# Performance work log

Hardware: AMD Instinct MI355X
Metric: run time of the kernel (lower is better)

## Reference

```python
import jax, jax.numpy as jnp
import numpy as np

B, T, D = 2, 2048, 1024
NH, NKV, HD = 16, 4, 64
KD = NKV * HD          # 256
PD = 16                # rope partial dim (rotated dims)
RANK = 8
ALPHA = 1.0
ROPE_BASE = 10000.0


def setup_inputs() -> dict:
    key = jax.random.key(0)
    ks = jax.random.split(key, 10)
    s = 0.02
    return {
        "x":      jax.random.normal(ks[0], (B, T, D), jnp.float32),
        "Wq":     jax.random.normal(ks[1], (D, D), jnp.float32) * s,
        "Wk":     jax.random.normal(ks[2], (KD, D), jnp.float32) * s,
        "Wv":     jax.random.normal(ks[3], (KD, D), jnp.float32) * s,
        "Wproj":  jax.random.normal(ks[4], (D, D), jnp.float32) * s,
        "q_gain": jnp.full((NH,), 5.25, jnp.float32),
        "Aq":     jax.random.normal(ks[5], (RANK, D), jnp.float32) * s,
        "Bq":     jax.random.normal(ks[6], (D, RANK), jnp.float32) * s,
        "Av":     jax.random.normal(ks[7], (RANK, D), jnp.float32) * s,
        "Bv":     jax.random.normal(ks[8], (KD, RANK), jnp.float32) * s,
    }


def _rms_norm(x):
    # F.rms_norm with no weight: x / sqrt(mean(x^2) + eps), eps = dtype machine eps
    eps = jnp.finfo(x.dtype).eps
    return x * jax.lax.rsqrt(jnp.mean(x * x, axis=-1, keepdims=True) + eps)


def _rope_partial(x, cos, sin, pd):
    # x: [B, T, H, HD]; rotate first pd dims (half/half), pass rest through
    h = pd // 2
    x1, x2, rest = x[..., :h], x[..., h:pd], x[..., pd:]
    c = cos[None, :, None, :]  # [1, T, 1, h]
    s = sin[None, :, None, :]
    return jnp.concatenate([x1 * c + x2 * s, -x2 * c + x1 * s, rest], axis=-1)


def reference(x, Wq, Wk, Wv, Wproj, q_gain, Aq, Bq, Av, Bv):
    # projections + per-step LoRA on Q and V (output = alpha * B(A(x)))
    q = x @ Wq.T + ALPHA * ((x @ Aq.T) @ Bq.T)          # [B,T,D]
    k = x @ Wk.T                                        # [B,T,KD]
    v = x @ Wv.T + ALPHA * ((x @ Av.T) @ Bv.T)          # [B,T,KD]

    q = _rms_norm(q.reshape(B, T, NH, HD))
    k = _rms_norm(k.reshape(B, T, NKV, HD))
    v = v.reshape(B, T, NKV, HD)

    # partial RoPE tables: [T, PD//2]
    inv = 1.0 / (ROPE_BASE ** (jnp.arange(0, PD, 2, dtype=jnp.float32) / PD))
    freqs = jnp.arange(T, dtype=jnp.float32)[:, None] * inv[None, :]
    cos, sin = jnp.cos(freqs), jnp.sin(freqs)
    q = _rope_partial(q, cos, sin, PD)
    k = _rope_partial(k, cos, sin, PD)

    # learned per-head QK gain on queries
    q = q * q_gain[None, None, :, None]

    # GQA: repeat-interleave kv heads to NH
    g = NH // NKV
    kf = jnp.repeat(k, g, axis=2)  # [B,T,NH,HD]
    vf = jnp.repeat(v, g, axis=2)

    scale = 1.0 / np.float32(np.sqrt(HD))
    scores = jnp.einsum('bqhd,bkhd->bhqk', q, kf) * scale  # [B,NH,T,T]
    causal = jnp.tril(jnp.ones((T, T), bool))
    scores = jnp.where(causal[None, None], scores, -jnp.inf)
    p = jax.nn.softmax(scores, axis=-1)
    y = jnp.einsum('bhqk,bkhd->bqhd', p, vf).reshape(B, T, D)
    return y @ Wproj.T
```

## Files before the change

kernel.cpp:

```cpp
#include <hip/hip_runtime.h>

#define Tn   2048
#define Dn   1024
#define KDn  256
#define NHn  16
#define NKVn 4
#define Rn   4096

typedef short bf16x8 __attribute__((ext_vector_type(8)));
typedef float f32x4  __attribute__((ext_vector_type(4)));
typedef const __attribute__((address_space(1))) unsigned* gas_p;
typedef __attribute__((address_space(3))) unsigned* las_p;

__device__ unsigned short g_q[(size_t)Rn * Dn];
__device__ unsigned short g_k[(size_t)Rn * KDn];
__device__ unsigned short g_vt[(size_t)2 * NKVn * 64 * Tn];
__device__ unsigned short g_y[(size_t)Rn * Dn];
__device__ unsigned short g_xb[(size_t)Rn * Dn];
__device__ unsigned short g_wq[(size_t)Dn * Dn];
__device__ unsigned short g_wk[(size_t)KDn * Dn];
__device__ unsigned short g_wv[(size_t)KDn * Dn];
__device__ unsigned short g_wp[(size_t)Dn * Dn];
__device__ float g_tq[Rn * 8];
__device__ float g_tv[Rn * 8];

static __device__ __forceinline__ float bf2f(unsigned short u) {
    return __uint_as_float(((unsigned)u) << 16);
}
static __device__ __forceinline__ unsigned short f2bf(float f) {
    unsigned u = __float_as_uint(f);
    u += 0x7fffu + ((u >> 16) & 1u);
    return (unsigned short)(u >> 16);
}
static __device__ __forceinline__ unsigned pk2bf(float a, float b) {
    return (unsigned)f2bf(a) | ((unsigned)f2bf(b) << 16);
}
static __device__ __forceinline__ unsigned cvtpk(float a, float b) {
    unsigned r;
    asm("v_cvt_pk_bf16_f32 %0, %1, %2" : "=v"(r) : "v"(a), "v"(b));
    return r;
}
static __device__ __forceinline__ float wave_sum(float s) {
    #pragma unroll
    for (int off = 32; off; off >>= 1) s += __shfl_xor(s, off);
    return s;
}

__global__ __launch_bounds__(256)
void lora_tmp(const float* __restrict__ x,
              const float* __restrict__ Aq,
              const float* __restrict__ Av) {
    int tid = threadIdx.x, wave = tid >> 6, lane = tid & 63;
    int row = blockIdx.x * 4 + wave;
    const float4* xr = (const float4*)(x + (size_t)row * Dn);
    uint2* xbo = (uint2*)g_xb + (size_t)row * (Dn / 4);
    float aq[8], av[8];
    #pragma unroll
    for (int r = 0; r < 8; r++) { aq[r] = 0.f; av[r] = 0.f; }
    for (int it = 0; it < Dn / 256; it++) {
        int j = it * 64 + lane;
        float4 xv = xr[j];
        xbo[j] = make_uint2(pk2bf(xv.x, xv.y), pk2bf(xv.z, xv.w));
        #pragma unroll
        for (int r = 0; r < 8; r++) {
            float4 a4 = ((const float4*)(Aq + (size_t)r * Dn))[j];
            aq[r] += xv.x * a4.x + xv.y * a4.y + xv.z * a4.z + xv.w * a4.w;
        }
        #pragma unroll
        for (int r = 0; r < 8; r++) {
            float4 a4 = ((const float4*)(Av + (size_t)r * Dn))[j];
            av[r] += xv.x * a4.x + xv.y * a4.y + xv.z * a4.z + xv.w * a4.w;
        }
    }
    #pragma unroll
    for (int r = 0; r < 8; r++) { aq[r] = wave_sum(aq[r]); av[r] = wave_sum(av[r]); }
    if (lane == 0) {
        #pragma unroll
        for (int r = 0; r < 8; r++) { g_tq[row * 8 + r] = aq[r]; g_tv[row * 8 + r] = av[r]; }
    }
}

#define NQ4 (Dn * Dn / 4)
#define NK4 (KDn * Dn / 4)
__global__ __launch_bounds__(256)
void cast_w(const float* __restrict__ Wq, const float* __restrict__ Wk,
            const float* __restrict__ Wv, const float* __restrict__ Wp) {
    int i = blockIdx.x * 256 + threadIdx.x;
    const float* src; unsigned short* dst; int o;
    if      (i < NQ4)                 { src = Wq; dst = g_wq; o = i; }
    else if (i < NQ4 + NK4)           { src = Wk; dst = g_wk; o = i - NQ4; }
    else if (i < NQ4 + 2 * NK4)       { src = Wv; dst = g_wv; o = i - NQ4 - NK4; }
    else                              { src = Wp; dst = g_wp; o = i - NQ4 - 2 * NK4; }
    float4 v = ((const float4*)src)[o];
    ((uint2*)dst)[o] = make_uint2(pk2bf(v.x, v.y), pk2bf(v.z, v.w));
}

template<int MODE>
__global__ __launch_bounds__(256, 2)
void gemm_bt(float* __restrict__ Cout, const float* __restrict__ BqL,
             const float* __restrict__ BvL, const float* __restrict__ qgain,
             int M, int K) {
    const unsigned short* A = (MODE == 0) ? g_xb : g_y;

    int gx = gridDim.x;
    int flat = blockIdx.y * gx + blockIdx.x;
    int cpx = (gx * gridDim.y) >> 3;
    int flat2 = (flat & 7) * cpx + (flat >> 3);
    int n0 = (flat2 % gx) * 64, m0 = (flat2 / gx) * 128;

    const unsigned short* W;
    int wroff, region;
    if (MODE == 0) {
        if (n0 < 1024)      { W = g_wq; wroff = n0;        region = 0; }
        else if (n0 < 1280) { W = g_wk; wroff = n0 - 1024; region = 1; }
        else                { W = g_wv; wroff = n0 - 1280; region = 2; }
    } else { W = g_wp; wroff = n0; region = 3; }

    __shared__ __align__(16) unsigned short SM[24576];
    int tid = threadIdx.x;
    int w = tid >> 6, lane = tid & 63;
    int m_ = lane & 15, quad = lane >> 4;

    int lrow = lane >> 3, lseg = (lane & 7) * 8;
    const unsigned short* agp[4];
    #pragma unroll
    for (int i = 0; i < 4; i++)
        agp[i] = A + (size_t)(m0 + w * 32 + i * 8 + lrow) * K + lseg;
    const unsigned short* wgp[2];
    #pragma unroll
    for (int i = 0; i < 2; i++)
        wgp[i] = W + (size_t)(wroff + w * 16 + i * 8 + lrow) * K + lseg;
    int alb[4], wlb[2];
    #pragma unroll
    for (int i = 0; i < 4; i++) alb[i] = (w * 32 + i * 8) * 64;
    #pragma unroll
    for (int i = 0; i < 2; i++) wlb[i] = 16384 + (w * 16 + i * 8) * 64;

    f32x4 acc[2][4];
    #pragma unroll
    for (int im = 0; im < 2; im++)
        #pragma unroll
        for (int in = 0; in < 4; in++) acc[im][in] = (f32x4){0.f, 0.f, 0.f, 0.f};

    #pragma unroll
    for (int i = 0; i < 4; i++)
        __builtin_amdgcn_global_load_lds((gas_p)agp[i], (las_p)&SM[alb[i]], 16, 0, 0);
    #pragma unroll
    for (int i = 0; i < 2; i++)
        __builtin_amdgcn_global_load_lds((gas_p)wgp[i], (las_p)&SM[wlb[i]], 16, 0, 0);

    int nk = K >> 6;
    for (int kt = 0; kt < nk; kt++) {
        __syncthreads();
        int cur = kt & 1, nxt = cur ^ 1;
        if (kt + 1 < nk) {
            int ko = (kt + 1) * 64;
            #pragma unroll
            for (int i = 0; i < 4; i++)
                __builtin_amdgcn_global_load_lds((gas_p)(agp[i] + ko),
                    (las_p)&SM[nxt * 8192 + alb[i]], 16, 0, 0);
            #pragma unroll
            for (int i = 0; i < 2; i++)
                __builtin_amdgcn_global_load_lds((gas_p)(wgp[i] + ko),
                    (las_p)&SM[wlb[i] + nxt * 4096], 16, 0, 0);
        }
        #pragma unroll
        for (int kk = 0; kk < 2; kk++) {
            bf16x8 bf[4];
            #pragma unroll
            for (int in = 0; in < 4; in++)
                bf[in] = *(const bf16x8*)&SM[16384 + cur * 4096 +
                                             (in * 16 + m_) * 64 + kk * 32 + quad * 8];
            #pragma unroll
            for (int im = 0; im < 2; im++) {
                bf16x8 af = *(const bf16x8*)&SM[cur * 8192 +
                                                (w * 32 + im * 16 + m_) * 64 + kk * 32 + quad * 8];
                #pragma unroll
                for (int in = 0; in < 4; in++)
                    acc[im][in] = __builtin_amdgcn_mfma_f32_16x16x32_bf16(af, bf[in], acc[im][in], 0, 0, 0);
            }
        }
    }

    if (MODE == 1) {
        #pragma unroll
        for (int im = 0; im < 2; im++)
            #pragma unroll
            for (int r = 0; r < 4; r++) {
                int row = m0 + w * 32 + im * 16 + quad * 4 + r;
                #pragma unroll
                for (int in = 0; in < 4; in++)
                    Cout[(size_t)row * Dn + (n0 + in * 16 + m_)] = acc[im][in][r];
            }
        return;
    }

    if (region <= 1) {
        float blc[4][8];
        if (region == 0) {
            #pragma unroll
            for (int in = 0; in < 4; in++) {
                const float* bp = BqL + (size_t)(n0 + in * 16 + m_) * 8;
                #pragma unroll
                for (int j = 0; j < 8; j++) blc[in][j] = bp[j];
            }
        }
        float ghead = (region == 0) ? qgain[n0 >> 6] * 0.18033688011112042f : 1.0f;
        #pragma unroll
        for (int im = 0; im < 2; im++) {
            #pragma unroll
            for (int r = 0; r < 4; r++) {
                int row = m0 + w * 32 + im * 16 + quad * 4 + r;
                float vv[4];
                float ss = 0.f;
                if (region == 0) {
                    const float* tp = g_tq + (size_t)row * 8;
                    float tv8[8];
                    #pragma unroll
                    for (int j = 0; j < 8; j++) tv8[j] = tp[j];
                    #pragma unroll
                    for (int in = 0; in < 4; in++) {
                        float val = acc[im][in][r];
                        #pragma unroll
                        for (int j = 0; j < 8; j++) val += tv8[j] * blc[in][j];
                        vv[in] = val; ss += val * val;
                    }
                } else {
                    #pragma unroll
                    for (int in = 0; in < 4; in++) { vv[in] = acc[im][in][r]; ss += vv[in] * vv[in]; }
                }
                ss += __shfl_xor(ss, 1); ss += __shfl_xor(ss, 2);
                ss += __shfl_xor(ss, 4); ss += __shfl_xor(ss, 8);
                float rs = rsqrtf(ss * (1.0f / 64.0f) + 1.1920929e-7f);
                #pragma unroll
                for (int in = 0; in < 4; in++) vv[in] *= rs;
                float p = __shfl_xor(vv[0], 8);
                int t = row & (Tn - 1);
                float fr = (float)t * exp2f(-(float)(m_ & 7) * 1.6609640474436813f);
                float c = cosf(fr), sn = sinf(fr);
                if (m_ < 16) vv[0] = (m_ < 8) ? vv[0] * c + p * sn : p * sn - vv[0] * c;
                #pragma unroll
                for (int in = 0; in < 4; in++) {
                    float val = vv[in] * ghead;
                    int col = n0 + in * 16 + m_;
                    if (region == 0) g_q[(size_t)row * Dn + col] = f2bf(val);
                    else             g_k[(size_t)row * KDn + (col - 1024)] = f2bf(val);
                }
            }
        }
    } else {
        float blc[4][8];
        #pragma unroll
        for (int in = 0; in < 4; in++) {
            const float* bp = BvL + (size_t)(n0 - 1280 + in * 16 + m_) * 8;
            #pragma unroll
            for (int j = 0; j < 8; j++) blc[in][j] = bp[j];
        }
        __syncthreads();
        #pragma unroll
        for (int im = 0; im < 2; im++) {
            #pragma unroll
            for (int r = 0; r < 4; r++) {
                int rl = w * 32 + im * 16 + quad * 4 + r;
                const float* tp = g_tv + (size_t)(m0 + rl) * 8;
                float tv8[8];
                #pragma unroll
                for (int j = 0; j < 8; j++) tv8[j] = tp[j];
                #pragma unroll
                for (int in = 0; in < 4; in++) {
                    float val = acc[im][in][r];
                    #pragma unroll
                    for (int j = 0; j < 8; j++) val += tv8[j] * blc[in][j];
                    SM[(in * 16 + m_) * 136 + rl] = f2bf(val);
                }
            }
        }
        __syncthreads();
        int d = tid >> 2, tseg = (tid & 3) * 32;
        int bb = m0 >> 11, t0 = m0 & (Tn - 1);
        int kvh = (n0 - 1280) >> 6;
        unsigned short* dst = g_vt + (((size_t)(bb * NKVn + kvh) * 64) + d) * Tn + t0 + tseg;
        const uint4* srcv = (const uint4*)&SM[d * 136 + tseg];
        uint4 c0 = srcv[0], c1 = srcv[1], c2 = srcv[2], c3 = srcv[3];
        ((uint4*)dst)[0] = c0; ((uint4*)dst)[1] = c1;
        ((uint4*)dst)[2] = c2; ((uint4*)dst)[3] = c3;
    }
}

__global__ __launch_bounds__(256, 4)
void attn_kernel() {
    __shared__ __align__(16) unsigned short KS[64 * 72];
    __shared__ __align__(16) unsigned short VS[64 * 72];
    __shared__ __align__(16) unsigned short Pt[4][16 * 72];
    int tid = threadIdx.x;
    int w = tid >> 6, lane = tid & 63;
    int q_ = lane & 15, quad = lane >> 4;
    int b = blockIdx.z, kvh = blockIdx.y, h = kvh * 4 + w;
    int bx = blockIdx.x;
    if ((kvh >> 1) & 1) bx = 127 - bx;
    int qb = bx * 16;
    int qg = qb + q_;

    const unsigned short* qrow =
        g_q + ((size_t)(b * Tn + qg) * NHn + h) * 64 + quad * 8;
    bf16x8 Qf0 = *(const bf16x8*)qrow;
    bf16x8 Qf1 = *(const bf16x8*)(qrow + 32);

    int srow = tid >> 2, sseg = (tid & 3) * 16;
    const unsigned short* kgp =
        g_k + ((size_t)(b * Tn + srow) * NKVn + kvh) * 64 + sseg;
    const unsigned short* vgp =
        g_vt + ((size_t)(b * NKVn + kvh) * 64 + srow) * Tn + sseg;

    f32x4 accO[4];
    #pragma unroll
    for (int i = 0; i < 4; i++) accO[i] = (f32x4){0.f, 0.f, 0.f, 0.f};
    float lsum = 0.f;
    int ntiles = (qb + 79) >> 6;

    {
        uint4 ka = *(const uint4*)kgp, kb = *(const uint4*)(kgp + 8);
        uint4 va = *(const uint4*)vgp, vb = *(const uint4*)(vgp + 8);
        *(uint4*)&KS[srow * 72 + sseg] = ka;
        *(uint4*)&KS[srow * 72 + sseg + 8] = kb;
        *(uint4*)&VS[srow * 72 + sseg] = va;
        *(uint4*)&VS[srow * 72 + sseg + 8] = vb;
    }
    __syncthreads();

    for (int kt = 0; kt < ntiles; kt++) {
        bool pre = (kt + 1 < ntiles);
        uint4 kan, kbn, van, vbn;
        if (pre) {
            const unsigned short* kp = kgp + (size_t)(kt + 1) * (64 * NKVn * 64);
            const unsigned short* vp = vgp + (kt + 1) * 64;
            kan = *(const uint4*)kp; kbn = *(const uint4*)(kp + 8);
            van = *(const uint4*)vp; vbn = *(const uint4*)(vp + 8);
        }

        f32x4 s[4];
        __builtin_amdgcn_s_setprio(1);
        #pragma unroll
        for (int ss = 0; ss < 4; ss++) {
            bf16x8 ka = *(const bf16x8*)&KS[(ss * 16 + q_) * 72 + quad * 8];
            bf16x8 kb = *(const bf16x8*)&KS[(ss * 16 + q_) * 72 + 32 + quad * 8];
            s[ss] = (f32x4){0.f, 0.f, 0.f, 0.f};
            s[ss] = __builtin_amdgcn_mfma_f32_16x16x32_bf16(ka, Qf0, s[ss], 0, 0, 0);
            s[ss] = __builtin_amdgcn_mfma_f32_16x16x32_bf16(kb, Qf1, s[ss], 0, 0, 0);
        }
        __builtin_amdgcn_s_setprio(0);

        if (kt == ntiles - 1) {
            #pragma unroll
            for (int ss = 0; ss < 4; ss++) {
                int k0 = kt * 64 + ss * 16 + quad * 4;
                #pragma unroll
                for (int r = 0; r < 4; r++)
                    if (k0 + r > qg) s[ss][r] = -1e30f;
            }
        }
        float p[4][4];
        #pragma unroll
        for (int ss = 0; ss < 4; ss++)
            #pragma unroll
            for (int r = 0; r < 4; r++) {
                p[ss][r] = exp2f(s[ss][r]);
                lsum += p[ss][r];
            }

        unsigned short* pb = &Pt[w][0];
        #pragma unroll
        for (int ss = 0; ss < 4; ss++)
            *(uint2*)&pb[q_ * 72 + ss * 16 + quad * 4] =
                make_uint2(cvtpk(p[ss][0], p[ss][1]), cvtpk(p[ss][2], p[ss][3]));
        bf16x8 pf0 = *(const bf16x8*)&pb[q_ * 72 + quad * 8];
        bf16x8 pf1 = *(const bf16x8*)&pb[q_ * 72 + 32 + quad * 8];

        __builtin_amdgcn_s_setprio(1);
        #pragma unroll
        for (int c = 0; c < 4; c++) {
            bf16x8 vf0 = *(const bf16x8*)&VS[(c * 16 + q_) * 72 + quad * 8];
            bf16x8 vf1 = *(const bf16x8*)&VS[(c * 16 + q_) * 72 + 32 + quad * 8];
            accO[c] = __builtin_amdgcn_mfma_f32_16x16x32_bf16(vf0, pf0, accO[c], 0, 0, 0);
            accO[c] = __builtin_amdgcn_mfma_f32_16x16x32_bf16(vf1, pf1, accO[c], 0, 0, 0);
        }
        __builtin_amdgcn_s_setprio(0);

        __syncthreads();
        if (pre) {
            *(uint4*)&KS[srow * 72 + sseg] = kan;
            *(uint4*)&KS[srow * 72 + sseg + 8] = kbn;
            *(uint4*)&VS[srow * 72 + sseg] = van;
            *(uint4*)&VS[srow * 72 + sseg + 8] = vbn;
        }
        __syncthreads();
    }

    lsum += __shfl_xor(lsum, 16);
    lsum += __shfl_xor(lsum, 32);
    float invl = 1.0f / lsum;
    unsigned short* yp = g_y + ((size_t)(b * Tn + qg) * NHn + h) * 64;
    #pragma unroll
    for (int c = 0; c < 4; c++) {
        uint2 o = make_uint2(cvtpk(accO[c][0] * invl, accO[c][1] * invl),
                             cvtpk(accO[c][2] * invl, accO[c][3] * invl));
        *(uint2*)&yp[c * 16 + quad * 4] = o;
    }
}

extern "C" void kernel_launch(void* const* d_in, const int* in_sizes, int n_in,
                              void* d_out, int out_size, void* d_ws, size_t ws_size,
                              hipStream_t stream) {
    const float* x  = (const float*)d_in[0];
    const float* Wq = (const float*)d_in[1];
    const float* Wk = (const float*)d_in[2];
    const float* Wv = (const float*)d_in[3];
    const float* Wp = (const float*)d_in[4];
    const float* qg = (const float*)d_in[5];
    const float* Aq = (const float*)d_in[6];
    const float* Bq = (const float*)d_in[7];
    const float* Av = (const float*)d_in[8];
    const float* Bv = (const float*)d_in[9];
    float* out = (float*)d_out;

    lora_tmp<<<dim3(Rn / 4), dim3(256), 0, stream>>>(x, Aq, Av);
    cast_w<<<dim3((NQ4 * 2 + NK4 * 2) / 256), dim3(256), 0, stream>>>(Wq, Wk, Wv, Wp);
    gemm_bt<0><<<dim3(1536 / 64, Rn / 128), dim3(256), 0, stream>>>(
        nullptr, Bq, Bv, qg, Rn, Dn);
    attn_kernel<<<dim3(Tn / 16, NKVn, 2), dim3(256), 0, stream>>>();
    gemm_bt<1><<<dim3(Dn / 64, Rn / 128), dim3(256), 0, stream>>>(
        out, nullptr, nullptr, nullptr, Rn, Dn);
}
```

Baseline: 189.4 us.

## Load K/V fragments directly from global memory, dropping shared-memory staging

The attention kernel no longer stages K and V tiles into shared memory with double-buffered register prefetch and two barriers per tile. Instead each wave loads its MFMA operand fragments for K and V straight from global memory, which is L2-cached and shared by the four heads in a KV group. This removes the block-wide synchronisation and the LDS traffic, but each wave now issues four times the global loads for the same K/V data. It also loses the explicit prefetch overlap, so global latency sits on the critical path unless the compiler or occupancy hides it.

Result: slower. 265.2 us (+40.0%).

```diff
diff --git a/kernel.cpp b/kernel.cpp
--- a/kernel.cpp
+++ b/kernel.cpp
@@ -289,8 +289,6 @@
 
 __global__ __launch_bounds__(256, 4)
 void attn_kernel() {
-    __shared__ __align__(16) unsigned short KS[64 * 72];
-    __shared__ __align__(16) unsigned short VS[64 * 72];
     __shared__ __align__(16) unsigned short Pt[4][16 * 72];
     int tid = threadIdx.x;
     int w = tid >> 6, lane = tid & 63;
@@ -306,11 +304,10 @@
     bf16x8 Qf0 = *(const bf16x8*)qrow;
     bf16x8 Qf1 = *(const bf16x8*)(qrow + 32);
 
-    int srow = tid >> 2, sseg = (tid & 3) * 16;
-    const unsigned short* kgp =
-        g_k + ((size_t)(b * Tn + srow) * NKVn + kvh) * 64 + sseg;
-    const unsigned short* vgp =
-        g_vt + ((size_t)(b * NKVn + kvh) * 64 + srow) * Tn + sseg;
+    const unsigned short* kbase =
+        g_k + ((size_t)(b * Tn + q_) * NKVn + kvh) * 64 + quad * 8;
+    const unsigned short* vbase =
+        g_vt + ((size_t)(b * NKVn + kvh) * 64 + q_) * Tn + quad * 8;
 
     f32x4 accO[4];
     #pragma unroll
@@ -318,37 +315,33 @@
     float lsum = 0.f;
     int ntiles = (qb + 79) >> 6;
 
-    {
-        uint4 ka = *(const uint4*)kgp, kb = *(const uint4*)(kgp + 8);
-        uint4 va = *(const uint4*)vgp, vb = *(const uint4*)(vgp + 8);
-        *(uint4*)&KS[srow * 72 + sseg] = ka;
-        *(uint4*)&KS[srow * 72 + sseg + 8] = kb;
-        *(uint4*)&VS[srow * 72 + sseg] = va;
-        *(uint4*)&VS[srow * 72 + sseg + 8] = vb;
-    }
-    __syncthreads();
-
     for (int kt = 0; kt < ntiles; kt++) {
-        bool pre = (kt + 1 < ntiles);
-        uint4 kan, kbn, van, vbn;
-        if (pre) {
-            const unsigned short* kp = kgp + (size_t)(kt + 1) * (64 * NKVn * 64);
-            const unsigned short* vp = vgp + (kt + 1) * 64;
-            kan = *(const uint4*)kp; kbn = *(const uint4*)(kp + 8);
-            van = *(const uint4*)vp; vbn = *(const uint4*)(vp + 8);
+        const unsigned short* kp = kbase + (size_t)(kt * 64) * (NKVn * 64);
+        bf16x8 ka[4], kb[4];
+        #pragma unroll
+        for (int ss = 0; ss < 4; ss++) {
+            const unsigned short* kr = kp + (size_t)(ss * 16) * (NKVn * 64);
+            ka[ss] = *(const bf16x8*)kr;
+            kb[ss] = *(const bf16x8*)(kr + 32);
         }
 
         f32x4 s[4];
         __builtin_amdgcn_s_setprio(1);
         #pragma unroll
         for (int ss = 0; ss < 4; ss++) {
-            bf16x8 ka = *(const bf16x8*)&KS[(ss * 16 + q_) * 72 + quad * 8];
-            bf16x8 kb = *(const bf16x8*)&KS[(ss * 16 + q_) * 72 + 32 + quad * 8];
             s[ss] = (f32x4){0.f, 0.f, 0.f, 0.f};
-            s[ss] = __builtin_amdgcn_mfma_f32_16x16x32_bf16(ka, Qf0, s[ss], 0, 0, 0);
-            s[ss] = __builtin_amdgcn_mfma_f32_16x16x32_bf16(kb, Qf1, s[ss], 0, 0, 0);
+            s[ss] = __builtin_amdgcn_mfma_f32_16x16x32_bf16(ka[ss], Qf0, s[ss], 0, 0, 0);
+            s[ss] = __builtin_amdgcn_mfma_f32_16x16x32_bf16(kb[ss], Qf1, s[ss], 0, 0, 0);
         }
         __builtin_amdgcn_s_setprio(0);
+
+        bf16x8 vf0[4], vf1[4];
+        #pragma unroll
+        for (int c = 0; c < 4; c++) {
+            const unsigned short* vp = vbase + (size_t)(c * 16) * Tn + kt * 64;
+            vf0[c] = *(const bf16x8*)vp;
+            vf1[c] = *(const bf16x8*)(vp + 32);
+        }
 
         if (kt == ntiles - 1) {
             #pragma unroll
@@ -379,21 +372,10 @@
         __builtin_amdgcn_s_setprio(1);
         #pragma unroll
         for (int c = 0; c < 4; c++) {
-            bf16x8 vf0 = *(const bf16x8*)&VS[(c * 16 + q_) * 72 + quad * 8];
-            bf16x8 vf1 = *(const bf16x8*)&VS[(c * 16 + q_) * 72 + 32 + quad * 8];
-            accO[c] = __builtin_amdgcn_mfma_f32_16x16x32_bf16(vf0, pf0, accO[c], 0, 0, 0);
-            accO[c] = __builtin_amdgcn_mfma_f32_16x16x32_bf16(vf1, pf1, accO[c], 0, 0, 0);
+            accO[c] = __builtin_amdgcn_mfma_f32_16x16x32_bf16(vf0[c], pf0, accO[c], 0, 0, 0);
+            accO[c] = __builtin_amdgcn_mfma_f32_16x16x32_bf16(vf1[c], pf1, accO[c], 0, 0, 0);
         }
         __builtin_amdgcn_s_setprio(0);
-
-        __syncthreads();
-        if (pre) {
-            *(uint4*)&KS[srow * 72 + sseg] = kan;
-            *(uint4*)&KS[srow * 72 + sseg + 8] = kbn;
-            *(uint4*)&VS[srow * 72 + sseg] = van;
-            *(uint4*)&VS[srow * 72 + sseg + 8] = vbn;
-        }
-        __syncthreads();
     }
 
     lsum += __shfl_xor(lsum, 16);
```
